# Performance work log

Measured on AMD Instinct MI355X. Metric: run time of the kernel, lower is better.

Reference implementation:

```python
import jax, jax.numpy as jnp
import numpy as np

D = 768
H = 12
EPS = 1e-5


def layer_norm(x, g, b):
    mu = jnp.mean(x, axis=-1, keepdims=True)
    var = jnp.var(x, axis=-1, keepdims=True)
    return (x - mu) * jax.lax.rsqrt(var + EPS) * g + b


def setup_inputs() -> dict:
    key = jax.random.key(0)
    ks = jax.random.split(key, 12)
    d, h = D, H
    x = jax.random.normal(ks[0], (4, 1024, d), dtype=jnp.float32)
    # attention projections (per-head dim is full d, per the module)
    s_qkv = (6.0 / (d + d * h)) ** 0.5  # xavier-like scale
    Wq = jax.random.uniform(ks[1], (d, d * h), jnp.float32, -s_qkv, s_qkv)
    Wk = jax.random.uniform(ks[2], (d, d * h), jnp.float32, -s_qkv, s_qkv)
    Wv = jax.random.uniform(ks[3], (d, d * h), jnp.float32, -s_qkv, s_qkv)
    Wu = jax.random.uniform(ks[4], (d * h, d), jnp.float32, -s_qkv, s_qkv)
    bu = jnp.zeros((d,), jnp.float32)
    # MLP
    s1 = (6.0 / (d + 4 * d)) ** 0.5
    W1 = jax.random.uniform(ks[5], (d, 4 * d), jnp.float32, -s1, s1)
    b1 = jax.random.normal(ks[6], (4 * d,), jnp.float32) * 1e-6
    W2 = jax.random.uniform(ks[7], (4 * d, d), jnp.float32, -s1, s1)
    b2 = jax.random.normal(ks[8], (d,), jnp.float32) * 1e-6
    ln1_g = jnp.ones((d,), jnp.float32)
    ln1_b = jnp.zeros((d,), jnp.float32)
    ln2_g = jnp.ones((d,), jnp.float32)
    ln2_b = jnp.zeros((d,), jnp.float32)
    return dict(x=x, Wq=Wq, Wk=Wk, Wv=Wv, Wu=Wu, bu=bu,
                ln1_g=ln1_g, ln1_b=ln1_b, ln2_g=ln2_g, ln2_b=ln2_b,
                W1=W1, b1=b1, W2=W2, b2=b2)


def reference(x, Wq, Wk, Wv, Wu, bu, ln1_g, ln1_b, ln2_g, ln2_b, W1, b1, W2, b2):
    b, n, d = x.shape
    h = H
    # --- pre-LN attention block ---
    res = x
    y = layer_norm(x, ln1_g, ln1_b)
    qs = (y @ Wq).reshape(b, n, h, d)  # per-head dim = d (module quirk)
    ks = (y @ Wk).reshape(b, n, h, d)
    vs = (y @ Wv).reshape(b, n, h, d)
    scores = jnp.einsum('bihd,bjhd->bhij', qs, ks) / (d ** 0.5)
    w = jax.nn.softmax(scores, axis=-1)
    att = jnp.einsum('bhij,bjhd->bihd', w, vs).reshape(b, n, h * d)
    y = att @ Wu + bu
    x = y + res
    # --- pre-LN MLP block (dropout is identity at inference) ---
    res = x
    y = layer_norm(x, ln2_g, ln2_b)
    y = jax.nn.relu(y @ W1 + b1)
    y = y @ W2 + b2
    return y + res
```

## Files before the change

### kernel.cpp

```cpp
#include <hip/hip_runtime.h>
#include <cstdint>
#include <cmath>


typedef __bf16 bf16_t;
typedef __bf16 bf16x8 __attribute__((ext_vector_type(8)));
typedef __bf16 bf16x4 __attribute__((ext_vector_type(4)));
typedef float floatx4 __attribute__((ext_vector_type(4)));

#define DMODEL 768
#define NHEAD  12
#define SEQ    1024
#define NBATCH 4
#define ROWS   (NBATCH*SEQ)
#define DH     (DMODEL*NHEAD)
#define DFF    (4*DMODEL)

template<bool BIAS, bool RES, bool RELU, int OMODE>
__global__ __launch_bounds__(256)
void gemm_v4(const bf16_t* __restrict__ A, const bf16_t* __restrict__ BT,
             void* __restrict__ Cv, int K, int lda, int ldb, int ldc,
             int bdiv, long sa_hi, long sa_lo, long sb_hi, long sb_lo,
             long sc_hi, long sc_lo,
             const float* __restrict__ bias, const float* __restrict__ res,
             int ldres, float alpha)
{
  __shared__ __align__(16) bf16_t As[128*32];
  __shared__ __align__(16) bf16_t Bs[128*32];

  const int tid  = threadIdx.x;
  const int wave = tid >> 6;
  const int lane = tid & 63;
  const int r    = lane & 15;
  const int q    = lane >> 4;

  const int z = blockIdx.z;
  A  += (long)(z / bdiv) * sa_hi + (long)(z % bdiv) * sa_lo;
  BT += (long)(z / bdiv) * sb_hi + (long)(z % bdiv) * sb_lo;
  const long coff = (long)(z / bdiv) * sc_hi + (long)(z % bdiv) * sc_lo;

  const int bm = blockIdx.y * 128;
  const int bn = blockIdx.x * 128;
  const int wm = (wave & 1) * 64;
  const int wn = (wave >> 1) * 64;

  const int blk0 = 2*wave, blk1 = 2*wave + 1;
  const bf16_t* a_src0 = A  + (long)(bm + blk0*16 + r) * lda + q*8;
  const bf16_t* a_src1 = A  + (long)(bm + blk1*16 + r) * lda + q*8;
  const bf16_t* b_src0 = BT + (long)(bn + blk0*16 + r) * ldb + q*8;
  const bf16_t* b_src1 = BT + (long)(bn + blk1*16 + r) * ldb + q*8;
  bf16_t* a_dst0 = As + blk0*512 + lane*8;
  bf16_t* a_dst1 = As + blk1*512 + lane*8;
  bf16_t* b_dst0 = Bs + blk0*512 + lane*8;
  bf16_t* b_dst1 = Bs + blk1*512 + lane*8;

  const int am = (wave & 1) * 4;
  const int bb = (wave >> 1) * 4;

  floatx4 acc[4][4] = {};

  for (int k0 = 0; k0 < K; k0 += 32) {
    bf16x8 av0 = *(const bf16x8*)(a_src0 + k0);
    bf16x8 av1 = *(const bf16x8*)(a_src1 + k0);
    bf16x8 bv0 = *(const bf16x8*)(b_src0 + k0);
    bf16x8 bv1 = *(const bf16x8*)(b_src1 + k0);
    *(bf16x8*)a_dst0 = av0;
    *(bf16x8*)a_dst1 = av1;
    *(bf16x8*)b_dst0 = bv0;
    *(bf16x8*)b_dst1 = bv1;
    __syncthreads();
    bf16x8 afrag[4], bfrag[4];
#pragma unroll
    for (int t = 0; t < 4; ++t) {
      afrag[t] = *(const bf16x8*)(As + (am + t)*512 + lane*8);
      bfrag[t] = *(const bf16x8*)(Bs + (bb + t)*512 + lane*8);
    }
#pragma unroll
    for (int mt = 0; mt < 4; ++mt)
#pragma unroll
      for (int nt = 0; nt < 4; ++nt)
        acc[mt][nt] = __builtin_amdgcn_mfma_f32_16x16x32_bf16(
            afrag[mt], bfrag[nt], acc[mt][nt], 0, 0, 0);
    __syncthreads();
  }

  const int row0 = bm + wm + q*4;
  const int col0 = bn + wn + r;
#pragma unroll
  for (int nt = 0; nt < 4; ++nt) {
    const int col = col0 + nt*16;
    float bv = 0.f;
    if (BIAS) bv = bias[col];
#pragma unroll
    for (int mt = 0; mt < 4; ++mt) {
#pragma unroll
      for (int e = 0; e < 4; ++e) {
        const int rowi = row0 + mt*16 + e;
        float v = acc[mt][nt][e] * alpha;
        if (BIAS) v += bv;
        if (RELU) v = fmaxf(v, 0.f);
        if (RES)  v += res[(long)rowi * ldres + col];
        const long idx = coff + (long)rowi * ldc + col;
        if (OMODE == 0)      ((bf16_t*)Cv)[idx] = (bf16_t)v;
        else if (OMODE == 1) ((float*)Cv)[idx] = v;
        else                 ((float*)Cv)[idx] += v;
      }
    }
  }
}

__global__ void tr_f2b_v4(const float* __restrict__ in, bf16_t* __restrict__ out,
                          int ldi, int ldo)
{
  __shared__ bf16_t tile[32][34];
  const int c0 = blockIdx.x * 32, r0 = blockIdx.y * 32;
  const int tx = threadIdx.x, ty = threadIdx.y;
#pragma unroll
  for (int i = 0; i < 4; ++i)
    tile[ty + 8*i][tx] = (bf16_t)in[(long)(r0 + ty + 8*i) * ldi + c0 + tx];
  __syncthreads();
#pragma unroll
  for (int i = 0; i < 4; ++i)
    out[(long)(c0 + ty + 8*i) * ldo + r0 + tx] = tile[tx][ty + 8*i];
}

__global__ void tr_b_v4(const bf16_t* __restrict__ in, bf16_t* __restrict__ out,
                        int ldi, int ldo, int bdiv,
                        long si_hi, long si_lo, long so_hi, long so_lo)
{
  __shared__ bf16_t tile[32][34];
  const int z = blockIdx.z;
  in  += (long)(z / bdiv) * si_hi + (long)(z % bdiv) * si_lo;
  out += (long)(z / bdiv) * so_hi + (long)(z % bdiv) * so_lo;
  const int c0 = blockIdx.x * 32, r0 = blockIdx.y * 32;
  const int tx = threadIdx.x, ty = threadIdx.y;
#pragma unroll
  for (int i = 0; i < 4; ++i)
    tile[ty + 8*i][tx] = in[(long)(r0 + ty + 8*i) * ldi + c0 + tx];
  __syncthreads();
#pragma unroll
  for (int i = 0; i < 4; ++i)
    out[(long)(c0 + ty + 8*i) * ldo + r0 + tx] = tile[tx][ty + 8*i];
}

__global__ void tr_wh_v4(const float* __restrict__ Wq, const float* __restrict__ Wk,
                         const float* __restrict__ Wv, const float* __restrict__ Wu,
                         bf16_t* __restrict__ WhT, bf16_t* __restrict__ WuTh, int h)
{
  __shared__ bf16_t tile[32][34];
  const int z = blockIdx.z;
  const float* in; bf16_t* out; int ldi;
  if (z < 3) {
    const float* W = (z == 0) ? Wq : (z == 1) ? Wk : Wv;
    in  = W + (long)h * DMODEL;
    ldi = DH;
    out = WhT + (long)z * DMODEL * DMODEL;
  } else {
    in  = Wu + (long)h * DMODEL * DMODEL;
    ldi = DMODEL;
    out = WuTh;
  }
  const int c0 = blockIdx.x * 32, r0 = blockIdx.y * 32;
  const int tx = threadIdx.x, ty = threadIdx.y;
#pragma unroll
  for (int i = 0; i < 4; ++i)
    tile[ty + 8*i][tx] = (bf16_t)in[(long)(r0 + ty + 8*i) * ldi + c0 + tx];
  __syncthreads();
#pragma unroll
  for (int i = 0; i < 4; ++i)
    out[(long)(c0 + ty + 8*i) * DMODEL + r0 + tx] = tile[tx][ty + 8*i];
}

__global__ void cast3_v4(const float* __restrict__ a, const float* __restrict__ b,
                         const float* __restrict__ c,
                         bf16_t* __restrict__ oa, bf16_t* __restrict__ ob,
                         bf16_t* __restrict__ oc)
{
  const float* src = (blockIdx.z == 0) ? a : (blockIdx.z == 1) ? b : c;
  bf16_t* dst      = (blockIdx.z == 0) ? oa : (blockIdx.z == 1) ? ob : oc;
  const long i = ((long)blockIdx.x * 256 + threadIdx.x) * 4;
  float4 v = *(const float4*)(src + i);
  bf16x4 o;
  o[0] = (bf16_t)v.x; o[1] = (bf16_t)v.y; o[2] = (bf16_t)v.z; o[3] = (bf16_t)v.w;
  *(bf16x4*)(dst + i) = o;
}

__global__ void cast1_v4(const float* __restrict__ src, bf16_t* __restrict__ dst)
{
  const long i = ((long)blockIdx.x * 256 + threadIdx.x) * 4;
  float4 v = *(const float4*)(src + i);
  bf16x4 o;
  o[0] = (bf16_t)v.x; o[1] = (bf16_t)v.y; o[2] = (bf16_t)v.z; o[3] = (bf16_t)v.w;
  *(bf16x4*)(dst + i) = o;
}

__global__ void ln_v4(const float* __restrict__ x, const float* __restrict__ g,
                      const float* __restrict__ b, bf16_t* __restrict__ y)
{
  const long row = blockIdx.x;
  const int tid = threadIdx.x;
  const float* xr = x + row * DMODEL;
  float v0 = xr[tid], v1 = xr[tid + 256], v2 = xr[tid + 512];
  float s  = v0 + v1 + v2;
  float ss = v0*v0 + v1*v1 + v2*v2;
  for (int o = 32; o; o >>= 1) { s += __shfl_down(s, o); ss += __shfl_down(ss, o); }
  __shared__ float rs[4], rss[4];
  const int wave = tid >> 6, lane = tid & 63;
  if (lane == 0) { rs[wave] = s; rss[wave] = ss; }
  __syncthreads();
  s  = rs[0] + rs[1] + rs[2] + rs[3];
  ss = rss[0] + rss[1] + rss[2] + rss[3];
  const float inv = 1.0f / (float)DMODEL;
  const float mean = s * inv;
  const float var  = ss * inv - mean * mean;
  const float rstd = rsqrtf(var + 1e-5f);
  bf16_t* yr = y + row * DMODEL;
  yr[tid]       = (bf16_t)(((v0 - mean) * rstd) * g[tid]       + b[tid]);
  yr[tid + 256] = (bf16_t)(((v1 - mean) * rstd) * g[tid + 256] + b[tid + 256]);
  yr[tid + 512] = (bf16_t)(((v2 - mean) * rstd) * g[tid + 512] + b[tid + 512]);
}

__global__ void softmax_v4(bf16_t* __restrict__ S)
{
  const long row = blockIdx.x;
  const int tid = threadIdx.x;
  bf16_t* p = S + row * SEQ + tid * 4;
  bf16x4 v = *(const bf16x4*)p;
  float f0 = (float)v[0], f1 = (float)v[1], f2 = (float)v[2], f3 = (float)v[3];
  float m = fmaxf(fmaxf(f0, f1), fmaxf(f2, f3));
  for (int o = 32; o; o >>= 1) m = fmaxf(m, __shfl_down(m, o));
  __shared__ float rm[4], rsum[4];
  const int wave = tid >> 6, lane = tid & 63;
  if (lane == 0) rm[wave] = m;
  __syncthreads();
  m = fmaxf(fmaxf(rm[0], rm[1]), fmaxf(rm[2], rm[3]));
  float e0 = __expf(f0 - m), e1 = __expf(f1 - m), e2 = __expf(f2 - m), e3 = __expf(f3 - m);
  float s = e0 + e1 + e2 + e3;
  for (int o = 32; o; o >>= 1) s += __shfl_down(s, o);
  if (lane == 0) rsum[wave] = s;
  __syncthreads();
  s = rsum[0] + rsum[1] + rsum[2] + rsum[3];
  const float invs = 1.0f / s;
  bf16x4 o4;
  o4[0] = (bf16_t)(e0 * invs); o4[1] = (bf16_t)(e1 * invs);
  o4[2] = (bf16_t)(e2 * invs); o4[3] = (bf16_t)(e3 * invs);
  *(bf16x4*)p = o4;
}

__global__ void finalize_v4(const float* __restrict__ acc, const float* __restrict__ add,
                            const float* __restrict__ bias, float* __restrict__ o)
{
  const long i = (long)blockIdx.x * 256 + threadIdx.x;
  const int c = (int)(i % DMODEL);
  o[i] = acc[i] + bias[c] + add[i];
}

template<int NP>
__global__ void reduce_v4(const float* __restrict__ p, const float* __restrict__ add,
                          const float* __restrict__ bias, float* __restrict__ o,
                          long plane)
{
  const long i = ((long)blockIdx.x * 256 + threadIdx.x) * 4;
  float4 s = *(const float4*)(p + i);
#pragma unroll
  for (int n = 1; n < NP; ++n) {
    float4 v = *(const float4*)(p + i + (long)n * plane);
    s.x += v.x; s.y += v.y; s.z += v.z; s.w += v.w;
  }
  const int c = (int)(i % DMODEL);
  float4 bv = *(const float4*)(bias + c);
  float4 av = *(const float4*)(add + i);
  float4 r;
  r.x = s.x + bv.x + av.x; r.y = s.y + bv.y + av.y;
  r.z = s.z + bv.z + av.z; r.w = s.w + bv.w + av.w;
  *(float4*)(o + i) = r;
}

extern "C" void kernel_launch(void* const* d_in, const int* in_sizes, int n_in,
                              void* d_out, int out_size, void* d_ws, size_t ws_size,
                              hipStream_t stream)
{
  (void)in_sizes; (void)n_in; (void)out_size;
  const float* x    = (const float*)d_in[0];
  const float* Wq   = (const float*)d_in[1];
  const float* Wk   = (const float*)d_in[2];
  const float* Wv   = (const float*)d_in[3];
  const float* Wu   = (const float*)d_in[4];
  const float* bu   = (const float*)d_in[5];
  const float* ln1g = (const float*)d_in[6];
  const float* ln1b = (const float*)d_in[7];
  const float* ln2g = (const float*)d_in[8];
  const float* ln2b = (const float*)d_in[9];
  const float* W1   = (const float*)d_in[10];
  const float* b1   = (const float*)d_in[11];
  const float* W2   = (const float*)d_in[12];
  const float* b2   = (const float*)d_in[13];
  float* out = (float*)d_out;

  char* ws = (char*)d_ws;
  size_t off = 0;
  auto alloc = [&](size_t bytes) -> void* {
    void* p = (void*)(ws + off);
    off += (bytes + 255) & ~(size_t)255;
    return p;
  };

  const float qk_alpha = 1.0f / sqrtf((float)DMODEL);
  dim3 tb(32, 8);

  const size_t SZ_W   = (size_t)DMODEL * DH * 2;
  const size_t SZ_MT  = (size_t)NHEAD * DMODEL * DMODEL * 2;
  const size_t SZ_Y   = (size_t)ROWS * DMODEL * 2;
  const size_t SZ_X2  = (size_t)ROWS * DMODEL * 4;

  if (ws_size >= (size_t)112e6) {
    bf16_t* MT  = (bf16_t*)alloc(SZ_MT);
    bf16_t* PhT = (bf16_t*)alloc(SZ_MT);
    bf16_t* y   = (bf16_t*)alloc(SZ_Y);
    float*  x2f = (float* )alloc(SZ_X2);
    char*   BIG = (char*  )alloc((size_t)62914560);
    bf16_t* T_b  = (bf16_t*)(BIG);
    bf16_t* S_b  = (bf16_t*)(BIG + 18874368);
    bf16_t* Zt_b = (bf16_t*)(BIG + 44040192);
    float*  part = (float* )(BIG);
    bf16_t* Wqb = (bf16_t*)(BIG);
    bf16_t* Wkb = (bf16_t*)(BIG + SZ_W);
    bf16_t* Wvb = (bf16_t*)(BIG + 2*SZ_W);
    bf16_t* WuT = (bf16_t*)(BIG + 3*SZ_W);
    bf16_t* W1T   = (bf16_t*)(BIG);
    bf16_t* W2T   = (bf16_t*)(BIG + 4718592);
    bf16_t* t     = (bf16_t*)(BIG + 9437184);
    float*  partM = (float* )(BIG + 34603008);
    bf16_t* y2    = y;

    cast3_v4<<<dim3(6912, 1, 3), 256, 0, stream>>>(Wq, Wk, Wv, Wqb, Wkb, Wvb);
    tr_f2b_v4<<<dim3(DMODEL/32, DH/32), tb, 0, stream>>>(Wu, WuT, DMODEL, DH);
    gemm_v4<false,false,false,0><<<dim3(6, 6, NHEAD), 256, 0, stream>>>(
        Wkb, Wqb, MT, DMODEL, DH, DH, DMODEL, NHEAD,
        0, DMODEL, 0, DMODEL, 0, (long)DMODEL*DMODEL, nullptr, nullptr, 0, 1.0f);
    gemm_v4<false,false,false,0><<<dim3(6, 6, NHEAD), 256, 0, stream>>>(
        WuT, Wvb, PhT, DMODEL, DH, DH, DMODEL, NHEAD,
        0, DMODEL, 0, DMODEL, 0, (long)DMODEL*DMODEL, nullptr, nullptr, 0, 1.0f);

    ln_v4<<<ROWS, 256, 0, stream>>>(x, ln1g, ln1b, y);
    for (int b = 0; b < NBATCH; ++b) {
      const bf16_t* yb = y + (long)b * SEQ * DMODEL;
      gemm_v4<false,false,false,0><<<dim3(6, 8, NHEAD), 256, 0, stream>>>(
          yb, MT, T_b, DMODEL, DMODEL, DMODEL, DMODEL, NHEAD,
          0, 0, 0, (long)DMODEL*DMODEL, 0, (long)SEQ*DMODEL,
          nullptr, nullptr, 0, 1.0f);
      gemm_v4<false,false,false,0><<<dim3(8, 8, NHEAD), 256, 0, stream>>>(
          T_b, yb, S_b, DMODEL, DMODEL, DMODEL, NHEAD*SEQ, NHEAD,
          0, (long)SEQ*DMODEL, 0, 0, 0, (long)SEQ,
          nullptr, nullptr, 0, qk_alpha);
      softmax_v4<<<NHEAD*SEQ, 256, 0, stream>>>(S_b);
      gemm_v4<false,false,false,0><<<dim3(8, 6, NHEAD), 256, 0, stream>>>(
          PhT, yb, Zt_b, DMODEL, DMODEL, DMODEL, NHEAD*SEQ, NHEAD,
          0, (long)DMODEL*DMODEL, 0, 0, 0, (long)SEQ,
          nullptr, nullptr, 0, 1.0f);
      gemm_v4<false,false,false,1><<<dim3(6, 8, 6), 256, 0, stream>>>(
          S_b, Zt_b, part, NHEAD*SEQ/6, NHEAD*SEQ, NHEAD*SEQ, DMODEL, 6,
          0, (long)(NHEAD*SEQ/6), 0, (long)(NHEAD*SEQ/6), 0, (long)SEQ*DMODEL,
          nullptr, nullptr, 0, 1.0f);
      reduce_v4<6><<<(SEQ*DMODEL)/1024, 256, 0, stream>>>(
          part, x + (long)b*SEQ*DMODEL, bu, x2f + (long)b*SEQ*DMODEL,
          (long)SEQ*DMODEL);
    }

    tr_f2b_v4<<<dim3(DFF/32, DMODEL/32), tb, 0, stream>>>(W1, W1T, DFF, DMODEL);
    tr_f2b_v4<<<dim3(DMODEL/32, DFF/32), tb, 0, stream>>>(W2, W2T, DMODEL, DFF);
    ln_v4<<<ROWS, 256, 0, stream>>>(x2f, ln2g, ln2b, y2);
    gemm_v4<true,false,true,0><<<dim3(DFF/128, ROWS/128, 1), 256, 0, stream>>>(
        y2, W1T, t, DMODEL, DMODEL, DMODEL, DFF, 1, 0,0,0,0,0,0, b1, nullptr, 0, 1.0f);
    gemm_v4<false,false,false,1><<<dim3(6, ROWS/128, 2), 256, 0, stream>>>(
        t, W2T, partM, DFF/2, DFF, DFF, DMODEL, 2,
        0, (long)(DFF/2), 0, (long)(DFF/2), 0, (long)ROWS*DMODEL,
        nullptr, nullptr, 0, 1.0f);
    reduce_v4<2><<<(ROWS*DMODEL)/1024, 256, 0, stream>>>(
        partM, x2f, b2, out, (long)ROWS*DMODEL);
  } else if (ws_size >= (size_t)70e6) {
    bf16_t* MT  = (bf16_t*)alloc(SZ_MT);
    bf16_t* PhT = (bf16_t*)alloc(SZ_MT);
    bf16_t* y   = (bf16_t*)alloc(SZ_Y);
    char*   R   = (char*  )alloc((size_t)33554432);
    bf16_t* WAb = (bf16_t*)(R);
    bf16_t* WBb = (bf16_t*)(R + SZ_W);
    float*  x2f = (float* )(R);
    bf16_t* T_h = (bf16_t*)(R + 12582912);
    bf16_t* S_h = (bf16_t*)(R + 18874368);
    bf16_t* Z_h = (bf16_t*)(R + 27262976);
    bf16_t* W1T = (bf16_t*)(R + 12582912);
    bf16_t* W2T = (bf16_t*)(R + 17301504);
    bf16_t* t   = (bf16_t*)MT;
    bf16_t* y2  = y;

    cast1_v4<<<6912, 256, 0, stream>>>(Wq, WAb);
    cast1_v4<<<6912, 256, 0, stream>>>(Wk, WBb);
    gemm_v4<false,false,false,0><<<dim3(6, 6, NHEAD), 256, 0, stream>>>(
        WBb, WAb, MT, DMODEL, DH, DH, DMODEL, NHEAD,
        0, DMODEL, 0, DMODEL, 0, (long)DMODEL*DMODEL, nullptr, nullptr, 0, 1.0f);
    cast1_v4<<<6912, 256, 0, stream>>>(Wv, WAb);
    tr_f2b_v4<<<dim3(DMODEL/32, DH/32), tb, 0, stream>>>(Wu, WBb, DMODEL, DH);
    gemm_v4<false,false,false,0><<<dim3(6, 6, NHEAD), 256, 0, stream>>>(
        WBb, WAb, PhT, DMODEL, DH, DH, DMODEL, NHEAD,
        0, DMODEL, 0, DMODEL, 0, (long)DMODEL*DMODEL, nullptr, nullptr, 0, 1.0f);

    ln_v4<<<ROWS, 256, 0, stream>>>(x, ln1g, ln1b, y);
    for (int h = 0; h < NHEAD; ++h) {
      const bf16_t* MTh  = MT  + (long)h * DMODEL * DMODEL;
      const bf16_t* PhTh = PhT + (long)h * DMODEL * DMODEL;
      gemm_v4<false,false,false,0><<<dim3(6, ROWS/128, 1), 256, 0, stream>>>(
          y, MTh, T_h, DMODEL, DMODEL, DMODEL, DMODEL, 1,
          0,0,0,0,0,0, nullptr, nullptr, 0, 1.0f);
      gemm_v4<false,false,false,0><<<dim3(8, 8, NBATCH), 256, 0, stream>>>(
          T_h, y, S_h, DMODEL, DMODEL, DMODEL, SEQ, NBATCH,
          0, (long)SEQ*DMODEL, 0, (long)SEQ*DMODEL, 0, (long)SEQ*SEQ,
          nullptr, nullptr, 0, qk_alpha);
      softmax_v4<<<ROWS, 256, 0, stream>>>(S_h);
      gemm_v4<false,false,false,0><<<dim3(8, 6, NBATCH), 256, 0, stream>>>(
          PhTh, y, Z_h, DMODEL, DMODEL, DMODEL, SEQ, NBATCH,
          0, 0, 0, (long)SEQ*DMODEL, 0, (long)DMODEL*SEQ,
          nullptr, nullptr, 0, 1.0f);
      if (h == 0)
        gemm_v4<false,false,false,1><<<dim3(6, 8, NBATCH), 256, 0, stream>>>(
            S_h, Z_h, x2f, SEQ, SEQ, SEQ, DMODEL, NBATCH,
            0, (long)SEQ*SEQ, 0, (long)DMODEL*SEQ, 0, (long)SEQ*DMODEL,
            nullptr, nullptr, 0, 1.0f);
      else
        gemm_v4<false,false,false,2><<<dim3(6, 8, NBATCH), 256, 0, stream>>>(
            S_h, Z_h, x2f, SEQ, SEQ, SEQ, DMODEL, NBATCH,
            0, (long)SEQ*SEQ, 0, (long)DMODEL*SEQ, 0, (long)SEQ*DMODEL,
            nullptr, nullptr, 0, 1.0f);
    }
    finalize_v4<<<(ROWS*DMODEL)/256, 256, 0, stream>>>(x2f, x, bu, x2f);

    tr_f2b_v4<<<dim3(DFF/32, DMODEL/32), tb, 0, stream>>>(W1, W1T, DFF, DMODEL);
    tr_f2b_v4<<<dim3(DMODEL/32, DFF/32), tb, 0, stream>>>(W2, W2T, DMODEL, DFF);
    ln_v4<<<ROWS, 256, 0, stream>>>(x2f, ln2g, ln2b, y2);
    gemm_v4<true,false,true,0><<<dim3(DFF/128, ROWS/128, 1), 256, 0, stream>>>(
        y2, W1T, t, DMODEL, DMODEL, DMODEL, DFF, 1, 0,0,0,0,0,0, b1, nullptr, 0, 1.0f);
    gemm_v4<true,true,false,1><<<dim3(6, ROWS/128, 1), 256, 0, stream>>>(
        t, W2T, out, DFF/2, DFF, DFF, DMODEL, 1, 0,0,0,0,0,0,
        b2, x2f, DMODEL, 1.0f);
    gemm_v4<false,false,false,2><<<dim3(6, ROWS/128, 1), 256, 0, stream>>>(
        t + DFF/2, W2T + DFF/2, out, DFF/2, DFF, DFF, DMODEL, 1, 0,0,0,0,0,0,
        nullptr, nullptr, 0, 1.0f);
  } else {
    bf16_t* W1T   = (bf16_t*)alloc((size_t)DMODEL * DFF * 2);
    bf16_t* W2T   = (bf16_t*)alloc((size_t)DMODEL * DFF * 2);
    bf16_t* y     = (bf16_t*)alloc(SZ_Y);
    float*  x2f   = (float* )alloc(SZ_X2);
    char*   reg1  = (char*)alloc((size_t)3*DMODEL*DMODEL*2 + (size_t)DMODEL*DMODEL*2 + (size_t)SEQ*DMODEL*2);
    bf16_t* WhT   = (bf16_t*)reg1;
    bf16_t* WuTh  = (bf16_t*)(reg1 + (size_t)3*DMODEL*DMODEL*2);
    bf16_t* attb  = (bf16_t*)(reg1 + (size_t)4*DMODEL*DMODEL*2);
    bf16_t* y2    = (bf16_t*)reg1;
    char*   reg2  = (char*)alloc((size_t)SEQ*3*DMODEL*2 + (size_t)DMODEL*SEQ*2 + (size_t)SEQ*SEQ*2);
    bf16_t* QKVb  = (bf16_t*)reg2;
    bf16_t* Vtb   = (bf16_t*)(reg2 + (size_t)SEQ*3*DMODEL*2);
    bf16_t* Sb    = (bf16_t*)(reg2 + (size_t)SEQ*3*DMODEL*2 + (size_t)DMODEL*SEQ*2);
    bf16_t* tslab = (bf16_t*)reg2;

    tr_f2b_v4<<<dim3(DFF/32, DMODEL/32), tb, 0, stream>>>(W1, W1T, DFF, DMODEL);
    tr_f2b_v4<<<dim3(DMODEL/32, DFF/32), tb, 0, stream>>>(W2, W2T, DMODEL, DFF);
    ln_v4<<<ROWS, 256, 0, stream>>>(x, ln1g, ln1b, y);

    const int N3 = 3 * DMODEL;
    for (int h = 0; h < NHEAD; ++h) {
      tr_wh_v4<<<dim3(24, 24, 4), tb, 0, stream>>>(Wq, Wk, Wv, Wu, WhT, WuTh, h);
      for (int b = 0; b < NBATCH; ++b) {
        const bf16_t* yb = y + (size_t)b * SEQ * DMODEL;
        gemm_v4<false,false,false,0><<<dim3(N3/128, SEQ/128, 1), 256, 0, stream>>>(
            yb, WhT, QKVb, DMODEL, DMODEL, DMODEL, N3, 1, 0,0,0,0,0,0,
            nullptr, nullptr, 0, 1.0f);
        tr_b_v4<<<dim3(DMODEL/32, SEQ/32, 1), tb, 0, stream>>>(
            QKVb + 2*DMODEL, Vtb, N3, SEQ, 1, 0,0,0,0);
        gemm_v4<false,false,false,0><<<dim3(SEQ/128, SEQ/128, 1), 256, 0, stream>>>(
            QKVb, QKVb + DMODEL, Sb, DMODEL, N3, N3, SEQ, 1, 0,0,0,0,0,0,
            nullptr, nullptr, 0, qk_alpha);
        softmax_v4<<<SEQ, 256, 0, stream>>>(Sb);
        gemm_v4<false,false,false,0><<<dim3(DMODEL/128, SEQ/128, 1), 256, 0, stream>>>(
            Sb, Vtb, attb, SEQ, SEQ, SEQ, DMODEL, 1, 0,0,0,0,0,0,
            nullptr, nullptr, 0, 1.0f);
        float* x2b = x2f + (size_t)b * SEQ * DMODEL;
        if (h == 0)
          gemm_v4<false,false,false,1><<<dim3(DMODEL/128, SEQ/128, 1), 256, 0, stream>>>(
              attb, WuTh, x2b, DMODEL, DMODEL, DMODEL, DMODEL, 1, 0,0,0,0,0,0,
              nullptr, nullptr, 0, 1.0f);
        else
          gemm_v4<false,false,false,2><<<dim3(DMODEL/128, SEQ/128, 1), 256, 0, stream>>>(
              attb, WuTh, x2b, DMODEL, DMODEL, DMODEL, DMODEL, 1, 0,0,0,0,0,0,
              nullptr, nullptr, 0, 1.0f);
      }
    }
    finalize_v4<<<(ROWS*DMODEL)/256, 256, 0, stream>>>(x2f, x, bu, x2f);
    ln_v4<<<ROWS, 256, 0, stream>>>(x2f, ln2g, ln2b, y2);
    for (int kb = 0; kb < 4; ++kb) {
      gemm_v4<true,false,true,0><<<dim3(DMODEL/128, ROWS/128, 1), 256, 0, stream>>>(
          y2, W1T + (size_t)kb*DMODEL*DMODEL, tslab, DMODEL, DMODEL, DMODEL, DMODEL, 1,
          0,0,0,0,0,0, b1 + kb*DMODEL, nullptr, 0, 1.0f);
      if (kb == 0)
        gemm_v4<true,true,false,1><<<dim3(DMODEL/128, ROWS/128, 1), 256, 0, stream>>>(
            tslab, W2T + (size_t)kb*DMODEL, out, DMODEL, DMODEL, DFF, DMODEL, 1,
            0,0,0,0,0,0, b2, x2f, DMODEL, 1.0f);
      else
        gemm_v4<false,false,false,2><<<dim3(DMODEL/128, ROWS/128, 1), 256, 0, stream>>>(
            tslab, W2T + (size_t)kb*DMODEL, out, DMODEL, DMODEL, DFF, DMODEL, 1,
            0,0,0,0,0,0, nullptr, nullptr, 0, 1.0f);
    }
  }
}
```

Baseline: 1.194 ms.

## Double GEMM K-tile to 64 and add batched all-batch attention path for large workspace

The GEMM kernel now stages a 64-wide K slice per iteration (two 32-wide sub-tiles) in shared memory, halving the number of barrier pairs per K loop. It also adds a new top branch for workspaces of 299e6 bytes or more. That branch batches the per-batch attention GEMMs, softmax and split-K reduction across all batches in single launches instead of a four-iteration loop. The cost is doubled LDS use per block and much larger intermediate buffers; whether the new branch runs depends on the workspace size the harness provides.

```diff
diff --git a/kernel.cpp b/kernel.cpp
--- a/kernel.cpp
+++ b/kernel.cpp
@@ -18,15 +18,15 @@
 
 template<bool BIAS, bool RES, bool RELU, int OMODE>
 __global__ __launch_bounds__(256)
-void gemm_v4(const bf16_t* __restrict__ A, const bf16_t* __restrict__ BT,
+void gemm_v6(const bf16_t* __restrict__ A, const bf16_t* __restrict__ BT,
              void* __restrict__ Cv, int K, int lda, int ldb, int ldc,
              int bdiv, long sa_hi, long sa_lo, long sb_hi, long sb_lo,
              long sc_hi, long sc_lo,
              const float* __restrict__ bias, const float* __restrict__ res,
              int ldres, float alpha)
 {
-  __shared__ __align__(16) bf16_t As[128*32];
-  __shared__ __align__(16) bf16_t Bs[128*32];
+  __shared__ __align__(16) bf16_t As[128*64];
+  __shared__ __align__(16) bf16_t Bs[128*64];
 
   const int tid  = threadIdx.x;
   const int wave = tid >> 6;
@@ -49,38 +49,47 @@
   const bf16_t* a_src1 = A  + (long)(bm + blk1*16 + r) * lda + q*8;
   const bf16_t* b_src0 = BT + (long)(bn + blk0*16 + r) * ldb + q*8;
   const bf16_t* b_src1 = BT + (long)(bn + blk1*16 + r) * ldb + q*8;
-  bf16_t* a_dst0 = As + blk0*512 + lane*8;
-  bf16_t* a_dst1 = As + blk1*512 + lane*8;
-  bf16_t* b_dst0 = Bs + blk0*512 + lane*8;
-  bf16_t* b_dst1 = Bs + blk1*512 + lane*8;
+  const int da0 = blk0*512 + lane*8;
+  const int da1 = blk1*512 + lane*8;
 
   const int am = (wave & 1) * 4;
   const int bb = (wave >> 1) * 4;
 
   floatx4 acc[4][4] = {};
 
-  for (int k0 = 0; k0 < K; k0 += 32) {
-    bf16x8 av0 = *(const bf16x8*)(a_src0 + k0);
-    bf16x8 av1 = *(const bf16x8*)(a_src1 + k0);
-    bf16x8 bv0 = *(const bf16x8*)(b_src0 + k0);
-    bf16x8 bv1 = *(const bf16x8*)(b_src1 + k0);
-    *(bf16x8*)a_dst0 = av0;
-    *(bf16x8*)a_dst1 = av1;
-    *(bf16x8*)b_dst0 = bv0;
-    *(bf16x8*)b_dst1 = bv1;
+  for (int k0 = 0; k0 < K; k0 += 64) {
+    bf16x8 a00 = *(const bf16x8*)(a_src0 + k0);
+    bf16x8 a01 = *(const bf16x8*)(a_src0 + k0 + 32);
+    bf16x8 a10 = *(const bf16x8*)(a_src1 + k0);
+    bf16x8 a11 = *(const bf16x8*)(a_src1 + k0 + 32);
+    bf16x8 b00 = *(const bf16x8*)(b_src0 + k0);
+    bf16x8 b01 = *(const bf16x8*)(b_src0 + k0 + 32);
+    bf16x8 b10 = *(const bf16x8*)(b_src1 + k0);
+    bf16x8 b11 = *(const bf16x8*)(b_src1 + k0 + 32);
+    *(bf16x8*)(As + da0)        = a00;
+    *(bf16x8*)(As + 4096 + da0) = a01;
+    *(bf16x8*)(As + da1)        = a10;
+    *(bf16x8*)(As + 4096 + da1) = a11;
+    *(bf16x8*)(Bs + da0)        = b00;
+    *(bf16x8*)(Bs + 4096 + da0) = b01;
+    *(bf16x8*)(Bs + da1)        = b10;
+    *(bf16x8*)(Bs + 4096 + da1) = b11;
     __syncthreads();
-    bf16x8 afrag[4], bfrag[4];
-#pragma unroll
-    for (int t = 0; t < 4; ++t) {
-      afrag[t] = *(const bf16x8*)(As + (am + t)*512 + lane*8);
-      bfrag[t] = *(const bf16x8*)(Bs + (bb + t)*512 + lane*8);
+#pragma unroll
+    for (int p = 0; p < 2; ++p) {
+      bf16x8 afrag[4], bfrag[4];
+#pragma unroll
+      for (int t = 0; t < 4; ++t) {
+        afrag[t] = *(const bf16x8*)(As + p*4096 + (am + t)*512 + lane*8);
+        bfrag[t] = *(const bf16x8*)(Bs + p*4096 + (bb + t)*512 + lane*8);
+      }
+#pragma unroll
+      for (int mt = 0; mt < 4; ++mt)
+#pragma unroll
+        for (int nt = 0; nt < 4; ++nt)
+          acc[mt][nt] = __builtin_amdgcn_mfma_f32_16x16x32_bf16(
+              afrag[mt], bfrag[nt], acc[mt][nt], 0, 0, 0);
     }
-#pragma unroll
-    for (int mt = 0; mt < 4; ++mt)
-#pragma unroll
-      for (int nt = 0; nt < 4; ++nt)
-        acc[mt][nt] = __builtin_amdgcn_mfma_f32_16x16x32_bf16(
-            afrag[mt], bfrag[nt], acc[mt][nt], 0, 0, 0);
     __syncthreads();
   }
 
@@ -109,7 +118,7 @@
   }
 }
 
-__global__ void tr_f2b_v4(const float* __restrict__ in, bf16_t* __restrict__ out,
+__global__ void tr_f2b_v6(const float* __restrict__ in, bf16_t* __restrict__ out,
                           int ldi, int ldo)
 {
   __shared__ bf16_t tile[32][34];
@@ -124,7 +133,7 @@
     out[(long)(c0 + ty + 8*i) * ldo + r0 + tx] = tile[tx][ty + 8*i];
 }
 
-__global__ void tr_b_v4(const bf16_t* __restrict__ in, bf16_t* __restrict__ out,
+__global__ void tr_b_v6(const bf16_t* __restrict__ in, bf16_t* __restrict__ out,
                         int ldi, int ldo, int bdiv,
                         long si_hi, long si_lo, long so_hi, long so_lo)
 {
@@ -143,7 +152,7 @@
     out[(long)(c0 + ty + 8*i) * ldo + r0 + tx] = tile[tx][ty + 8*i];
 }
 
-__global__ void tr_wh_v4(const float* __restrict__ Wq, const float* __restrict__ Wk,
+__global__ void tr_wh_v6(const float* __restrict__ Wq, const float* __restrict__ Wk,
                          const float* __restrict__ Wv, const float* __restrict__ Wu,
                          bf16_t* __restrict__ WhT, bf16_t* __restrict__ WuTh, int h)
 {
@@ -171,7 +180,7 @@
     out[(long)(c0 + ty + 8*i) * DMODEL + r0 + tx] = tile[tx][ty + 8*i];
 }
 
-__global__ void cast3_v4(const float* __restrict__ a, const float* __restrict__ b,
+__global__ void cast3_v6(const float* __restrict__ a, const float* __restrict__ b,
                          const float* __restrict__ c,
                          bf16_t* __restrict__ oa, bf16_t* __restrict__ ob,
                          bf16_t* __restrict__ oc)
@@ -185,7 +194,7 @@
   *(bf16x4*)(dst + i) = o;
 }
 
-__global__ void cast1_v4(const float* __restrict__ src, bf16_t* __restrict__ dst)
+__global__ void cast1_v6(const float* __restrict__ src, bf16_t* __restrict__ dst)
 {
   const long i = ((long)blockIdx.x * 256 + threadIdx.x) * 4;
   float4 v = *(const float4*)(src + i);
@@ -194,7 +203,7 @@
   *(bf16x4*)(dst + i) = o;
 }
 
-__global__ void ln_v4(const float* __restrict__ x, const float* __restrict__ g,
+__global__ void ln_v6(const float* __restrict__ x, const float* __restrict__ g,
                       const float* __restrict__ b, bf16_t* __restrict__ y)
 {
   const long row = blockIdx.x;
@@ -220,7 +229,7 @@
   yr[tid + 512] = (bf16_t)(((v2 - mean) * rstd) * g[tid + 512] + b[tid + 512]);
 }
 
-__global__ void softmax_v4(bf16_t* __restrict__ S)
+__global__ void softmax_v6(bf16_t* __restrict__ S)
 {
   const long row = blockIdx.x;
   const int tid = threadIdx.x;
@@ -247,7 +256,7 @@
   *(bf16x4*)p = o4;
 }
 
-__global__ void finalize_v4(const float* __restrict__ acc, const float* __restrict__ add,
+__global__ void finalize_v6(const float* __restrict__ acc, const float* __restrict__ add,
                             const float* __restrict__ bias, float* __restrict__ o)
 {
   const long i = (long)blockIdx.x * 256 + threadIdx.x;
@@ -256,7 +265,7 @@
 }
 
 template<int NP>
-__global__ void reduce_v4(const float* __restrict__ p, const float* __restrict__ add,
+__global__ void reduce_v6(const float* __restrict__ p, const float* __restrict__ add,
                           const float* __restrict__ bias, float* __restrict__ o,
                           long plane)
 {
@@ -313,7 +322,68 @@
   const size_t SZ_Y   = (size_t)ROWS * DMODEL * 2;
   const size_t SZ_X2  = (size_t)ROWS * DMODEL * 4;
 
-  if (ws_size >= (size_t)112e6) {
+  if (ws_size >= (size_t)299e6) {
+    bf16_t* MT   = (bf16_t*)alloc(SZ_MT);
+    bf16_t* PhT  = (bf16_t*)alloc(SZ_MT);
+    bf16_t* y    = (bf16_t*)alloc(SZ_Y);
+    float*  x2f  = (float* )alloc(SZ_X2);
+    bf16_t* T    = (bf16_t*)alloc((size_t)NBATCH * NHEAD * SEQ * DMODEL * 2);
+    bf16_t* S    = (bf16_t*)alloc((size_t)NBATCH * SEQ * NHEAD * SEQ * 2);
+    bf16_t* Zt   = (bf16_t*)alloc((size_t)NBATCH * DMODEL * NHEAD * SEQ * 2);
+    bf16_t* Wqb  = (bf16_t*)T;
+    bf16_t* Wkb  = (bf16_t*)((char*)T + SZ_W);
+    bf16_t* Wvb  = (bf16_t*)((char*)T + 2*SZ_W);
+    bf16_t* WuT  = (bf16_t*)((char*)T + 3*SZ_W);
+    float*  part = (float*)T;
+    bf16_t* W1T  = (bf16_t*)S;
+    bf16_t* W2T  = (bf16_t*)((char*)S + 4718592);
+    bf16_t* t    = (bf16_t*)((char*)S + 9437184);
+    float*  partM= (float* )((char*)S + 34603008);
+    bf16_t* y2   = (bf16_t*)Zt;
+
+    cast3_v6<<<dim3(6912, 1, 3), 256, 0, stream>>>(Wq, Wk, Wv, Wqb, Wkb, Wvb);
+    tr_f2b_v6<<<dim3(DMODEL/32, DH/32), tb, 0, stream>>>(Wu, WuT, DMODEL, DH);
+    gemm_v6<false,false,false,0><<<dim3(6, 6, NHEAD), 256, 0, stream>>>(
+        Wkb, Wqb, MT, DMODEL, DH, DH, DMODEL, NHEAD,
+        0, DMODEL, 0, DMODEL, 0, (long)DMODEL*DMODEL, nullptr, nullptr, 0, 1.0f);
+    gemm_v6<false,false,false,0><<<dim3(6, 6, NHEAD), 256, 0, stream>>>(
+        WuT, Wvb, PhT, DMODEL, DH, DH, DMODEL, NHEAD,
+        0, DMODEL, 0, DMODEL, 0, (long)DMODEL*DMODEL, nullptr, nullptr, 0, 1.0f);
+
+    ln_v6<<<ROWS, 256, 0, stream>>>(x, ln1g, ln1b, y);
+    gemm_v6<false,false,false,0><<<dim3(6, 8, NBATCH*NHEAD), 256, 0, stream>>>(
+        y, MT, T, DMODEL, DMODEL, DMODEL, DMODEL, NHEAD,
+        (long)SEQ*DMODEL, 0, 0, (long)DMODEL*DMODEL,
+        (long)NHEAD*SEQ*DMODEL, (long)SEQ*DMODEL, nullptr, nullptr, 0, 1.0f);
+    gemm_v6<false,false,false,0><<<dim3(8, 8, NBATCH*NHEAD), 256, 0, stream>>>(
+        T, y, S, DMODEL, DMODEL, DMODEL, NHEAD*SEQ, NHEAD,
+        (long)NHEAD*SEQ*DMODEL, (long)SEQ*DMODEL, (long)SEQ*DMODEL, 0,
+        (long)SEQ*NHEAD*SEQ, (long)SEQ, nullptr, nullptr, 0, qk_alpha);
+    softmax_v6<<<NBATCH*SEQ*NHEAD, 256, 0, stream>>>(S);
+    gemm_v6<false,false,false,0><<<dim3(8, 6, NBATCH*NHEAD), 256, 0, stream>>>(
+        PhT, y, Zt, DMODEL, DMODEL, DMODEL, NHEAD*SEQ, NHEAD,
+        0, (long)DMODEL*DMODEL, (long)SEQ*DMODEL, 0,
+        (long)DMODEL*NHEAD*SEQ, (long)SEQ, nullptr, nullptr, 0, 1.0f);
+    gemm_v6<false,false,false,1><<<dim3(6, 8, 24), 256, 0, stream>>>(
+        S, Zt, part, NHEAD*SEQ/6, NHEAD*SEQ, NHEAD*SEQ, DMODEL, NBATCH,
+        (long)(NHEAD*SEQ/6), (long)SEQ*NHEAD*SEQ,
+        (long)(NHEAD*SEQ/6), (long)DMODEL*NHEAD*SEQ,
+        (long)ROWS*DMODEL, (long)SEQ*DMODEL, nullptr, nullptr, 0, 1.0f);
+    reduce_v6<6><<<(ROWS*DMODEL)/1024, 256, 0, stream>>>(
+        part, x, bu, x2f, (long)ROWS*DMODEL);
+
+    tr_f2b_v6<<<dim3(DFF/32, DMODEL/32), tb, 0, stream>>>(W1, W1T, DFF, DMODEL);
+    tr_f2b_v6<<<dim3(DMODEL/32, DFF/32), tb, 0, stream>>>(W2, W2T, DMODEL, DFF);
+    ln_v6<<<ROWS, 256, 0, stream>>>(x2f, ln2g, ln2b, y2);
+    gemm_v6<true,false,true,0><<<dim3(DFF/128, ROWS/128, 1), 256, 0, stream>>>(
+        y2, W1T, t, DMODEL, DMODEL, DMODEL, DFF, 1, 0,0,0,0,0,0, b1, nullptr, 0, 1.0f);
+    gemm_v6<false,false,false,1><<<dim3(6, ROWS/128, 2), 256, 0, stream>>>(
+        t, W2T, partM, DFF/2, DFF, DFF, DMODEL, 2,
+        0, (long)(DFF/2), 0, (long)(DFF/2), 0, (long)ROWS*DMODEL,
+        nullptr, nullptr, 0, 1.0f);
+    reduce_v6<2><<<(ROWS*DMODEL)/1024, 256, 0, stream>>>(
+        partM, x2f, b2, out, (long)ROWS*DMODEL);
+  } else if (ws_size >= (size_t)112e6) {
     bf16_t* MT  = (bf16_t*)alloc(SZ_MT);
     bf16_t* PhT = (bf16_t*)alloc(SZ_MT);
     bf16_t* y   = (bf16_t*)alloc(SZ_Y);
@@ -333,50 +403,50 @@
     float*  partM = (float* )(BIG + 34603008);
     bf16_t* y2    = y;
 
-    cast3_v4<<<dim3(6912, 1, 3), 256, 0, stream>>>(Wq, Wk, Wv, Wqb, Wkb, Wvb);
-    tr_f2b_v4<<<dim3(DMODEL/32, DH/32), tb, 0, stream>>>(Wu, WuT, DMODEL, DH);
-    gemm_v4<false,false,false,0><<<dim3(6, 6, NHEAD), 256, 0, stream>>>(
+    cast3_v6<<<dim3(6912, 1, 3), 256, 0, stream>>>(Wq, Wk, Wv, Wqb, Wkb, Wvb);
+    tr_f2b_v6<<<dim3(DMODEL/32, DH/32), tb, 0, stream>>>(Wu, WuT, DMODEL, DH);
+    gemm_v6<false,false,false,0><<<dim3(6, 6, NHEAD), 256, 0, stream>>>(
         Wkb, Wqb, MT, DMODEL, DH, DH, DMODEL, NHEAD,
         0, DMODEL, 0, DMODEL, 0, (long)DMODEL*DMODEL, nullptr, nullptr, 0, 1.0f);
-    gemm_v4<false,false,false,0><<<dim3(6, 6, NHEAD), 256, 0, stream>>>(
+    gemm_v6<false,false,false,0><<<dim3(6, 6, NHEAD), 256, 0, stream>>>(
         WuT, Wvb, PhT, DMODEL, DH, DH, DMODEL, NHEAD,
         0, DMODEL, 0, DMODEL, 0, (long)DMODEL*DMODEL, nullptr, nullptr, 0, 1.0f);
 
-    ln_v4<<<ROWS, 256, 0, stream>>>(x, ln1g, ln1b, y);
+    ln_v6<<<ROWS, 256, 0, stream>>>(x, ln1g, ln1b, y);
     for (int b = 0; b < NBATCH; ++b) {
       const bf16_t* yb = y + (long)b * SEQ * DMODEL;
-      gemm_v4<false,false,false,0><<<dim3(6, 8, NHEAD), 256, 0, stream>>>(
+      gemm_v6<false,false,false,0><<<dim3(6, 8, NHEAD), 256, 0, stream>>>(
           yb, MT, T_b, DMODEL, DMODEL, DMODEL, DMODEL, NHEAD,
           0, 0, 0, (long)DMODEL*DMODEL, 0, (long)SEQ*DMODEL,
           nullptr, nullptr, 0, 1.0f);
-      gemm_v4<false,false,false,0><<<dim3(8, 8, NHEAD), 256, 0, stream>>>(
+      gemm_v6<false,false,false,0><<<dim3(8, 8, NHEAD), 256, 0, stream>>>(
           T_b, yb, S_b, DMODEL, DMODEL, DMODEL, NHEAD*SEQ, NHEAD,
           0, (long)SEQ*DMODEL, 0, 0, 0, (long)SEQ,
           nullptr, nullptr, 0, qk_alpha);
-      softmax_v4<<<NHEAD*SEQ, 256, 0, stream>>>(S_b);
-      gemm_v4<false,false,false,0><<<dim3(8, 6, NHEAD), 256, 0, stream>>>(
+      softmax_v6<<<NHEAD*SEQ, 256, 0, stream>>>(S_b);
+      gemm_v6<false,false,false,0><<<dim3(8, 6, NHEAD), 256, 0, stream>>>(
           PhT, yb, Zt_b, DMODEL, DMODEL, DMODEL, NHEAD*SEQ, NHEAD,
           0, (long)DMODEL*DMODEL, 0, 0, 0, (long)SEQ,
           nullptr, nullptr, 0, 1.0f);
-      gemm_v4<false,false,false,1><<<dim3(6, 8, 6), 256, 0, stream>>>(
+      gemm_v6<false,false,false,1><<<dim3(6, 8, 6), 256, 0, stream>>>(
           S_b, Zt_b, part, NHEAD*SEQ/6, NHEAD*SEQ, NHEAD*SEQ, DMODEL, 6,
           0, (long)(NHEAD*SEQ/6), 0, (long)(NHEAD*SEQ/6), 0, (long)SEQ*DMODEL,
           nullptr, nullptr, 0, 1.0f);
-      reduce_v4<6><<<(SEQ*DMODEL)/1024, 256, 0, stream>>>(
+      reduce_v6<6><<<(SEQ*DMODEL)/1024, 256, 0, stream>>>(
           part, x + (long)b*SEQ*DMODEL, bu, x2f + (long)b*SEQ*DMODEL,
           (long)SEQ*DMODEL);
     }
 
-    tr_f2b_v4<<<dim3(DFF/32, DMODEL/32), tb, 0, stream>>>(W1, W1T, DFF, DMODEL);
-    tr_f2b_v4<<<dim3(DMODEL/32, DFF/32), tb, 0, stream>>>(W2, W2T, DMODEL, DFF);
-    ln_v4<<<ROWS, 256, 0, stream>>>(x2f, ln2g, ln2b, y2);
-    gemm_v4<true,false,true,0><<<dim3(DFF/128, ROWS/128, 1), 256, 0, stream>>>(
+    tr_f2b_v6<<<dim3(DFF/32, DMODEL/32), tb, 0, stream>>>(W1, W1T, DFF, DMODEL);
+    tr_f2b_v6<<<dim3(DMODEL/32, DFF/32), tb, 0, stream>>>(W2, W2T, DMODEL, DFF);
+    ln_v6<<<ROWS, 256, 0, stream>>>(x2f, ln2g, ln2b, y2);
+    gemm_v6<true,false,true,0><<<dim3(DFF/128, ROWS/128, 1), 256, 0, stream>>>(
         y2, W1T, t, DMODEL, DMODEL, DMODEL, DFF, 1, 0,0,0,0,0,0, b1, nullptr, 0, 1.0f);
-    gemm_v4<false,false,false,1><<<dim3(6, ROWS/128, 2), 256, 0, stream>>>(
+    gemm_v6<false,false,false,1><<<dim3(6, ROWS/128, 2), 256, 0, stream>>>(
         t, W2T, partM, DFF/2, DFF, DFF, DMODEL, 2,
         0, (long)(DFF/2), 0, (long)(DFF/2), 0, (long)ROWS*DMODEL,
         nullptr, nullptr, 0, 1.0f);
-    reduce_v4<2><<<(ROWS*DMODEL)/1024, 256, 0, stream>>>(
+    reduce_v6<2><<<(ROWS*DMODEL)/1024, 256, 0, stream>>>(
         partM, x2f, b2, out, (long)ROWS*DMODEL);
   } else if (ws_size >= (size_t)70e6) {
     bf16_t* MT  = (bf16_t*)alloc(SZ_MT);
@@ -394,55 +464,55 @@
     bf16_t* t   = (bf16_t*)MT;
     bf16_t* y2  = y;
 
-    cast1_v4<<<6912, 256, 0, stream>>>(Wq, WAb);
-    cast1_v4<<<6912, 256, 0, stream>>>(Wk, WBb);
-    gemm_v4<false,false,false,0><<<dim3(6, 6, NHEAD), 256, 0, stream>>>(
+    cast1_v6<<<6912, 256, 0, stream>>>(Wq, WAb);
+    cast1_v6<<<6912, 256, 0, stream>>>(Wk, WBb);
+    gemm_v6<false,false,false,0><<<dim3(6, 6, NHEAD), 256, 0, stream>>>(
         WBb, WAb, MT, DMODEL, DH, DH, DMODEL, NHEAD,
         0, DMODEL, 0, DMODEL, 0, (long)DMODEL*DMODEL, nullptr, nullptr, 0, 1.0f);
-    cast1_v4<<<6912, 256, 0, stream>>>(Wv, WAb);
-    tr_f2b_v4<<<dim3(DMODEL/32, DH/32), tb, 0, stream>>>(Wu, WBb, DMODEL, DH);
-    gemm_v4<false,false,false,0><<<dim3(6, 6, NHEAD), 256, 0, stream>>>(
+    cast1_v6<<<6912, 256, 0, stream>>>(Wv, WAb);
+    tr_f2b_v6<<<dim3(DMODEL/32, DH/32), tb, 0, stream>>>(Wu, WBb, DMODEL, DH);
+    gemm_v6<false,false,false,0><<<dim3(6, 6, NHEAD), 256, 0, stream>>>(
         WBb, WAb, PhT, DMODEL, DH, DH, DMODEL, NHEAD,
         0, DMODEL, 0, DMODEL, 0, (long)DMODEL*DMODEL, nullptr, nullptr, 0, 1.0f);
 
-    ln_v4<<<ROWS, 256, 0, stream>>>(x, ln1g, ln1b, y);
+    ln_v6<<<ROWS, 256, 0, stream>>>(x, ln1g, ln1b, y);
     for (int h = 0; h < NHEAD; ++h) {
       const bf16_t* MTh  = MT  + (long)h * DMODEL * DMODEL;
       const bf16_t* PhTh = PhT + (long)h * DMODEL * DMODEL;
-      gemm_v4<false,false,false,0><<<dim3(6, ROWS/128, 1), 256, 0, stream>>>(
+      gemm_v6<false,false,false,0><<<dim3(6, ROWS/128, 1), 256, 0, stream>>>(
           y, MTh, T_h, DMODEL, DMODEL, DMODEL, DMODEL, 1,
           0,0,0,0,0,0, nullptr, nullptr, 0, 1.0f);
-      gemm_v4<false,false,false,0><<<dim3(8, 8, NBATCH), 256, 0, stream>>>(
+      gemm_v6<false,false,false,0><<<dim3(8, 8, NBATCH), 256, 0, stream>>>(
           T_h, y, S_h, DMODEL, DMODEL, DMODEL, SEQ, NBATCH,
           0, (long)SEQ*DMODEL, 0, (long)SEQ*DMODEL, 0, (long)SEQ*SEQ,
           nullptr, nullptr, 0, qk_alpha);
-      softmax_v4<<<ROWS, 256, 0, stream>>>(S_h);
-      gemm_v4<false,false,false,0><<<dim3(8, 6, NBATCH), 256, 0, stream>>>(
+      softmax_v6<<<ROWS, 256, 0, stream>>>(S_h);
+      gemm_v6<false,false,false,0><<<dim3(8, 6, NBATCH), 256, 0, stream>>>(
           PhTh, y, Z_h, DMODEL, DMODEL, DMODEL, SEQ, NBATCH,
           0, 0, 0, (long)SEQ*DMODEL, 0, (long)DMODEL*SEQ,
           nullptr, nullptr, 0, 1.0f);
       if (h == 0)
-        gemm_v4<false,false,false,1><<<dim3(6, 8, NBATCH), 256, 0, stream>>>(
+        gemm_v6<false,false,false,1><<<dim3(6, 8, NBATCH), 256, 0, stream>>>(
             S_h, Z_h, x2f, SEQ, SEQ, SEQ, DMODEL, NBATCH,
             0, (long)SEQ*SEQ, 0, (long)DMODEL*SEQ, 0, (long)SEQ*DMODEL,
             nullptr, nullptr, 0, 1.0f);
       else
-        gemm_v4<false,false,false,2><<<dim3(6, 8, NBATCH), 256, 0, stream>>>(
+        gemm_v6<false,false,false,2><<<dim3(6, 8, NBATCH), 256, 0, stream>>>(
             S_h, Z_h, x2f, SEQ, SEQ, SEQ, DMODEL, NBATCH,
             0, (long)SEQ*SEQ, 0, (long)DMODEL*SEQ, 0, (long)SEQ*DMODEL,
             nullptr, nullptr, 0, 1.0f);
     }
-    finalize_v4<<<(ROWS*DMODEL)/256, 256, 0, stream>>>(x2f, x, bu, x2f);
-
-    tr_f2b_v4<<<dim3(DFF/32, DMODEL/32), tb, 0, stream>>>(W1, W1T, DFF, DMODEL);
-    tr_f2b_v4<<<dim3(DMODEL/32, DFF/32), tb, 0, stream>>>(W2, W2T, DMODEL, DFF);
-    ln_v4<<<ROWS, 256, 0, stream>>>(x2f, ln2g, ln2b, y2);
-    gemm_v4<true,false,true,0><<<dim3(DFF/128, ROWS/128, 1), 256, 0, stream>>>(
+    finalize_v6<<<(ROWS*DMODEL)/256, 256, 0, stream>>>(x2f, x, bu, x2f);
+
+    tr_f2b_v6<<<dim3(DFF/32, DMODEL/32), tb, 0, stream>>>(W1, W1T, DFF, DMODEL);
+    tr_f2b_v6<<<dim3(DMODEL/32, DFF/32), tb, 0, stream>>>(W2, W2T, DMODEL, DFF);
+    ln_v6<<<ROWS, 256, 0, stream>>>(x2f, ln2g, ln2b, y2);
+    gemm_v6<true,false,true,0><<<dim3(DFF/128, ROWS/128, 1), 256, 0, stream>>>(
         y2, W1T, t, DMODEL, DMODEL, DMODEL, DFF, 1, 0,0,0,0,0,0, b1, nullptr, 0, 1.0f);
-    gemm_v4<true,true,false,1><<<dim3(6, ROWS/128, 1), 256, 0, stream>>>(
+    gemm_v6<true,true,false,1><<<dim3(6, ROWS/128, 1), 256, 0, stream>>>(
         t, W2T, out, DFF/2, DFF, DFF, DMODEL, 1, 0,0,0,0,0,0,
         b2, x2f, DMODEL, 1.0f);
-    gemm_v4<false,false,false,2><<<dim3(6, ROWS/128, 1), 256, 0, stream>>>(
+    gemm_v6<false,false,false,2><<<dim3(6, ROWS/128, 1), 256, 0, stream>>>(
         t + DFF/2, W2T + DFF/2, out, DFF/2, DFF, DFF, DMODEL, 1, 0,0,0,0,0,0,
         nullptr, nullptr, 0, 1.0f);
   } else {
@@ -461,50 +531,50 @@
     bf16_t* Sb    = (bf16_t*)(reg2 + (size_t)SEQ*3*DMODEL*2 + (size_t)DMODEL*SEQ*2);
     bf16_t* tslab = (bf16_t*)reg2;
 
-    tr_f2b_v4<<<dim3(DFF/32, DMODEL/32), tb, 0, stream>>>(W1, W1T, DFF, DMODEL);
-    tr_f2b_v4<<<dim3(DMODEL/32, DFF/32), tb, 0, stream>>>(W2, W2T, DMODEL, DFF);
-    ln_v4<<<ROWS, 256, 0, stream>>>(x, ln1g, ln1b, y);
+    tr_f2b_v6<<<dim3(DFF/32, DMODEL/32), tb, 0, stream>>>(W1, W1T, DFF, DMODEL);
+    tr_f2b_v6<<<dim3(DMODEL/32, DFF/32), tb, 0, stream>>>(W2, W2T, DMODEL, DFF);
+    ln_v6<<<ROWS, 256, 0, stream>>>(x, ln1g, ln1b, y);
 
     const int N3 = 3 * DMODEL;
     for (int h = 0; h < NHEAD; ++h) {
-      tr_wh_v4<<<dim3(24, 24, 4), tb, 0, stream>>>(Wq, Wk, Wv, Wu, WhT, WuTh, h);
+      tr_wh_v6<<<dim3(24, 24, 4), tb, 0, stream>>>(Wq, Wk, Wv, Wu, WhT, WuTh, h);
       for (int b = 0; b < NBATCH; ++b) {
         const bf16_t* yb = y + (size_t)b * SEQ * DMODEL;
-        gemm_v4<false,false,false,0><<<dim3(N3/128, SEQ/128, 1), 256, 0, stream>>>(
+        gemm_v6<false,false,false,0><<<dim3(N3/128, SEQ/128, 1), 256, 0, stream>>>(
             yb, WhT, QKVb, DMODEL, DMODEL, DMODEL, N3, 1, 0,0,0,0,0,0,
             nullptr, nullptr, 0, 1.0f);
-        tr_b_v4<<<dim3(DMODEL/32, SEQ/32, 1), tb, 0, stream>>>(
+        tr_b_v6<<<dim3(DMODEL/32, SEQ/32, 1), tb, 0, stream>>>(
             QKVb + 2*DMODEL, Vtb, N3, SEQ, 1, 0,0,0,0);
-        gemm_v4<false,false,false,0><<<dim3(SEQ/128, SEQ/128, 1), 256, 0, stream>>>(
+        gemm_v6<false,false,false,0><<<dim3(SEQ/128, SEQ/128, 1), 256, 0, stream>>>(
             QKVb, QKVb + DMODEL, Sb, DMODEL, N3, N3, SEQ, 1, 0,0,0,0,0,0,
             nullptr, nullptr, 0, qk_alpha);
-        softmax_v4<<<SEQ, 256, 0, stream>>>(Sb);
-        gemm_v4<false,false,false,0><<<dim3(DMODEL/128, SEQ/128, 1), 256, 0, stream>>>(
+        softmax_v6<<<SEQ, 256, 0, stream>>>(Sb);
+        gemm_v6<false,false,false,0><<<dim3(DMODEL/128, SEQ/128, 1), 256, 0, stream>>>(
             Sb, Vtb, attb, SEQ, SEQ, SEQ, DMODEL, 1, 0,0,0,0,0,0,
             nullptr, nullptr, 0, 1.0f);
         float* x2b = x2f + (size_t)b * SEQ * DMODEL;
         if (h == 0)
-          gemm_v4<false,false,false,1><<<dim3(DMODEL/128, SEQ/128, 1), 256, 0, stream>>>(
+          gemm_v6<false,false,false,1><<<dim3(DMODEL/128, SEQ/128, 1), 256, 0, stream>>>(
               attb, WuTh, x2b, DMODEL, DMODEL, DMODEL, DMODEL, 1, 0,0,0,0,0,0,
               nullptr, nullptr, 0, 1.0f);
         else
-          gemm_v4<false,false,false,2><<<dim3(DMODEL/128, SEQ/128, 1), 256, 0, stream>>>(
+          gemm_v6<false,false,false,2><<<dim3(DMODEL/128, SEQ/128, 1), 256, 0, stream>>>(
               attb, WuTh, x2b, DMODEL, DMODEL, DMODEL, DMODEL, 1, 0,0,0,0,0,0,
               nullptr, nullptr, 0, 1.0f);
       }
     }
-    finalize_v4<<<(ROWS*DMODEL)/256, 256, 0, stream>>>(x2f, x, bu, x2f);
-    ln_v4<<<ROWS, 256, 0, stream>>>(x2f, ln2g, ln2b, y2);
+    finalize_v6<<<(ROWS*DMODEL)/256, 256, 0, stream>>>(x2f, x, bu, x2f);
+    ln_v6<<<ROWS, 256, 0, stream>>>(x2f, ln2g, ln2b, y2);
     for (int kb = 0; kb < 4; ++kb) {
-      gemm_v4<true,false,true,0><<<dim3(DMODEL/128, ROWS/128, 1), 256, 0, stream>>>(
+      gemm_v6<true,false,true,0><<<dim3(DMODEL/128, ROWS/128, 1), 256, 0, stream>>>(
           y2, W1T + (size_t)kb*DMODEL*DMODEL, tslab, DMODEL, DMODEL, DMODEL, DMODEL, 1,
           0,0,0,0,0,0, b1 + kb*DMODEL, nullptr, 0, 1.0f);
       if (kb == 0)
-        gemm_v4<true,true,false,1><<<dim3(DMODEL/128, ROWS/128, 1), 256, 0, stream>>>(
+        gemm_v6<true,true,false,1><<<dim3(DMODEL/128, ROWS/128, 1), 256, 0, stream>>>(
             tslab, W2T + (size_t)kb*DMODEL, out, DMODEL, DMODEL, DFF, DMODEL, 1,
             0,0,0,0,0,0, b2, x2f, DMODEL, 1.0f);
       else
-        gemm_v4<false,false,false,2><<<dim3(DMODEL/128, ROWS/128, 1), 256, 0, stream>>>(
+        gemm_v6<false,false,false,2><<<dim3(DMODEL/128, ROWS/128, 1), 256, 0, stream>>>(
             tslab, W2T + (size_t)kb*DMODEL, out, DMODEL, DMODEL, DFF, DMODEL, 1,
             0,0,0,0,0,0, nullptr, nullptr, 0, 1.0f);
     }
```

After: 1.170 ms. -2.0%, faster.
